# Performance work log

Hardware: AMD Instinct MI355X
Metric: run time of the kernel (lower is better)

The kernel has to match this reference:

```python
import jax, jax.numpy as jnp
import numpy as np

N_NODES = 200000


def gcn_conv(x, src, dst, W, b, num_nodes):
    # PyG GCNConv: add self-loops, symmetric deg^-1/2 normalization,
    # message = norm * (x W)[src], aggregate = scatter-add onto dst, + bias.
    h = x @ W  # [N, out]
    loop = jnp.arange(num_nodes, dtype=src.dtype)
    s = jnp.concatenate([src, loop])
    d = jnp.concatenate([dst, loop])
    deg = jax.ops.segment_sum(jnp.ones_like(d, dtype=h.dtype), d, num_segments=num_nodes)
    dinv = jnp.where(deg > 0, jax.lax.rsqrt(deg), 0.0)
    norm = dinv[s] * dinv[d]  # [E+N]
    msg = h[s] * norm[:, None]  # gather + scale
    out = jax.ops.segment_sum(msg, d, num_segments=num_nodes)  # scatter-add
    return out + b


def setup_inputs() -> dict:
    key = jax.random.key(0)
    k1, k2, k3, k4, k5 = jax.random.split(key, 5)
    x = jax.random.normal(k1, (N_NODES, 3), dtype=jnp.float32)
    edge_index = jax.random.randint(k2, (2, 6400000), 0, N_NODES, dtype=jnp.int64)
    # Glorot-style init for GCN weights, zero bias (PyG defaults)
    W1 = jax.random.normal(k3, (3, 16), dtype=jnp.float32) * (1.0 / np.sqrt(3.0))
    b1 = jnp.zeros((16,), dtype=jnp.float32)
    W2 = jax.random.normal(k4, (16, 1), dtype=jnp.float32) * (1.0 / np.sqrt(16.0))
    b2 = jnp.zeros((1,), dtype=jnp.float32)
    return {"x": x, "edge_index": edge_index, "W1": W1, "b1": b1, "W2": W2, "b2": b2}


def reference(x, edge_index, W1, b1, W2, b2):
    src, dst = edge_index[0], edge_index[1]
    h = gcn_conv(x, src, dst, W1, b1, N_NODES)
    h = jax.nn.relu(h)
    return gcn_conv(h, src, dst, W2, b2, N_NODES)
```

## Files before the change

kernel.cpp:

```cpp
#include <hip/hip_runtime.h>

#define BLK 256
#define PSH 11
#define PART 2048
#define GHB 1024
#define MAXB 256
#define S1SCALE 2097152.0f
#define S2SCALE 524288.0f


__device__ __forceinline__ int edge_at(const void* idx, int is64, long long pos) {
  return is64 ? (int)((const long long*)idx)[pos] : ((const int*)idx)[pos];
}

__global__ void k_detect(const unsigned* __restrict__ w, int* __restrict__ flag) {
  __shared__ int any;
  if (threadIdx.x == 0) any = 0;
  __syncthreads();
  if (w[2 * threadIdx.x + 1] != 0u) atomicOr(&any, 1);
  __syncthreads();
  if (threadIdx.x == 0) *flag = (any == 0) ? 1 : 0;
}


__global__ __launch_bounds__(BLK) void k_hist(const void* __restrict__ ei,
                                              const int* __restrict__ flag,
                                              int E, int chunk, int NB,
                                              int* __restrict__ hist) {
  __shared__ int cnt[MAXB];
  for (int j = threadIdx.x; j < NB; j += BLK) cnt[j] = 0;
  __syncthreads();
  int is64 = *flag;
  int beg = blockIdx.x * chunk, end = min(E, beg + chunk);
  int i = beg + (int)threadIdx.x;
  for (; i + 3 * BLK < end; i += 4 * BLK) {
    int d0 = edge_at(ei, is64, (long long)E + i);
    int d1 = edge_at(ei, is64, (long long)E + i + BLK);
    int d2 = edge_at(ei, is64, (long long)E + i + 2 * BLK);
    int d3 = edge_at(ei, is64, (long long)E + i + 3 * BLK);
    atomicAdd(&cnt[d0 >> PSH], 1);
    atomicAdd(&cnt[d1 >> PSH], 1);
    atomicAdd(&cnt[d2 >> PSH], 1);
    atomicAdd(&cnt[d3 >> PSH], 1);
  }
  for (; i < end; i += BLK)
    atomicAdd(&cnt[edge_at(ei, is64, (long long)E + i) >> PSH], 1);
  __syncthreads();
  int* row = hist + (size_t)blockIdx.x * NB;
  for (int j = threadIdx.x; j < NB; j += BLK) row[j] = cnt[j];
}

__global__ __launch_bounds__(BLK) void k_scan1(int* __restrict__ hist, int NB,
                                               int* __restrict__ btot) {
  const int R = GHB / BLK;
  __shared__ int sd[BLK];
  int b = blockIdx.x, t = threadIdx.x;
  int v[R];
  int sum = 0;
#pragma unroll
  for (int r = 0; r < R; ++r) {
    v[r] = hist[(size_t)(t * R + r) * NB + b];
    sum += v[r];
  }
  sd[t] = sum;
  __syncthreads();
  for (int off = 1; off < BLK; off <<= 1) {
    int tmp = (t >= off) ? sd[t - off] : 0;
    __syncthreads();
    sd[t] += tmp;
    __syncthreads();
  }
  int run = sd[t] - sum;
#pragma unroll
  for (int r = 0; r < R; ++r) {
    int tmp = v[r];
    hist[(size_t)(t * R + r) * NB + b] = run;
    run += tmp;
  }
  if (t == BLK - 1) btot[b] = run;
}

__global__ void k_scan2(const int* __restrict__ btot, int NB, int* __restrict__ ebstart) {
  __shared__ int s[MAXB];
  for (int j = threadIdx.x; j < NB; j += blockDim.x) s[j] = btot[j];
  __syncthreads();
  if (threadIdx.x == 0) {
    int run = 0;
    for (int j = 0; j < NB; ++j) { ebstart[j] = run; run += s[j]; }
    ebstart[NB] = run;
  }
}

__global__ __launch_bounds__(BLK) void k_part(const void* __restrict__ ei,
                                              const int* __restrict__ flag,
                                              int E, int chunk, int NB,
                                              const int* __restrict__ offs,
                                              const int* __restrict__ ebstart,
                                              int* __restrict__ packed) {
  __shared__ int cnt[MAXB];
  int t = threadIdx.x;
  if (t < NB) cnt[t] = ebstart[t] + offs[(size_t)blockIdx.x * NB + t];
  __syncthreads();
  int is64 = *flag;
  int beg = blockIdx.x * chunk, end = min(E, beg + chunk);
  int i = beg + t;
  for (; i + 3 * BLK < end; i += 4 * BLK) {
    int s0 = edge_at(ei, is64, i);
    int s1 = edge_at(ei, is64, i + BLK);
    int s2 = edge_at(ei, is64, i + 2 * BLK);
    int s3 = edge_at(ei, is64, i + 3 * BLK);
    int d0 = edge_at(ei, is64, (long long)E + i);
    int d1 = edge_at(ei, is64, (long long)E + i + BLK);
    int d2 = edge_at(ei, is64, (long long)E + i + 2 * BLK);
    int d3 = edge_at(ei, is64, (long long)E + i + 3 * BLK);
    int p0 = atomicAdd(&cnt[d0 >> PSH], 1);
    int p1 = atomicAdd(&cnt[d1 >> PSH], 1);
    int p2 = atomicAdd(&cnt[d2 >> PSH], 1);
    int p3 = atomicAdd(&cnt[d3 >> PSH], 1);
    packed[p0] = (s0 << PSH) | (d0 & (PART - 1));
    packed[p1] = (s1 << PSH) | (d1 & (PART - 1));
    packed[p2] = (s2 << PSH) | (d2 & (PART - 1));
    packed[p3] = (s3 << PSH) | (d3 & (PART - 1));
  }
  for (; i < end; i += BLK) {
    int s = edge_at(ei, is64, i);
    int d = edge_at(ei, is64, (long long)E + i);
    int pos = atomicAdd(&cnt[d >> PSH], 1);
    packed[pos] = (s << PSH) | (d & (PART - 1));
  }
}

#define SLICE_BOUNDS(KB_)                                                     \
  int b = blockIdx.x, k = blockIdx.y;                                         \
  int s0 = ebstart[b], len = ebstart[b + 1] - s0;                             \
  int lo = s0 + (int)((long long)len * k / (KB_));                            \
  int hi = s0 + (int)((long long)len * (k + 1) / (KB_));                      \
  int alo = min((lo + 3) & ~3, hi);                                           \
  int nvec = (hi - alo) & ~3;                                                 \
  int tails = alo + nvec;

__global__ __launch_bounds__(BLK) void k_degb(const int* __restrict__ packed,
                                              const int* __restrict__ ebstart,
                                              int N, int DKB, int* __restrict__ degp) {
  __shared__ int cnt[PART];
  for (int j = threadIdx.x; j < PART; j += BLK) cnt[j] = 0;
  __syncthreads();
  SLICE_BOUNDS(DKB)
  int t = threadIdx.x;
  if (t < alo - lo) atomicAdd(&cnt[packed[lo + t] & (PART - 1)], 1);
  for (int base = alo + t * 4; base < tails; base += BLK * 4) {
    int4 q = *(const int4*)(packed + base);
    atomicAdd(&cnt[q.x & (PART - 1)], 1);
    atomicAdd(&cnt[q.y & (PART - 1)], 1);
    atomicAdd(&cnt[q.z & (PART - 1)], 1);
    atomicAdd(&cnt[q.w & (PART - 1)], 1);
  }
  if (t < hi - tails) atomicAdd(&cnt[packed[tails + t] & (PART - 1)], 1);
  __syncthreads();
  int pstart = b << PSH;
  int psize = min(N - pstart, PART);
  int* out = degp + (size_t)k * N + pstart;
  for (int j = threadIdx.x; j < psize; j += BLK) out[j] = cnt[j];
}

__global__ __launch_bounds__(BLK) void k_prepb(const int* __restrict__ degp, int DKB,
                                               int N, const float* __restrict__ x,
                                               int4* __restrict__ gx4i) {
  int n = blockIdx.x * blockDim.x + threadIdx.x;
  if (n >= N) return;
  int deg = 1;
  for (int k = 0; k < DKB; ++k) deg += degp[(size_t)k * N + n];
  float di = rsqrtf((float)deg);
  int4 g;
  g.x = __float2int_rn(di * x[3 * n + 0] * S1SCALE);
  g.y = __float2int_rn(di * x[3 * n + 1] * S1SCALE);
  g.z = __float2int_rn(di * x[3 * n + 2] * S1SCALE);
  g.w = __float_as_int(di);
  gx4i[n] = g;
}

__global__ __launch_bounds__(BLK) void k_s1b(const int* __restrict__ packed,
                                             const int* __restrict__ ebstart,
                                             int N, int S1KB,
                                             const int4* __restrict__ gx4i,
                                             int* __restrict__ p1) {
  __shared__ int acc[3 * PART];
  for (int j = threadIdx.x; j < 3 * PART; j += BLK) acc[j] = 0;
  __syncthreads();
  SLICE_BOUNDS(S1KB)
  int t = threadIdx.x;
  if (t < alo - lo) {
    int e = packed[lo + t];
    int4 g = gx4i[e >> PSH];
    int a = 3 * (e & (PART - 1));
    atomicAdd(&acc[a + 0], g.x);
    atomicAdd(&acc[a + 1], g.y);
    atomicAdd(&acc[a + 2], g.z);
  }
  for (int base = alo + t * 4; base < tails; base += BLK * 4) {
    int4 q = *(const int4*)(packed + base);
    int4 g0 = gx4i[q.x >> PSH];
    int4 g1 = gx4i[q.y >> PSH];
    int4 g2 = gx4i[q.z >> PSH];
    int4 g3 = gx4i[q.w >> PSH];
    int a0 = 3 * (q.x & (PART - 1)), a1 = 3 * (q.y & (PART - 1));
    int a2 = 3 * (q.z & (PART - 1)), a3 = 3 * (q.w & (PART - 1));
    atomicAdd(&acc[a0 + 0], g0.x);
    atomicAdd(&acc[a0 + 1], g0.y);
    atomicAdd(&acc[a0 + 2], g0.z);
    atomicAdd(&acc[a1 + 0], g1.x);
    atomicAdd(&acc[a1 + 1], g1.y);
    atomicAdd(&acc[a1 + 2], g1.z);
    atomicAdd(&acc[a2 + 0], g2.x);
    atomicAdd(&acc[a2 + 1], g2.y);
    atomicAdd(&acc[a2 + 2], g2.z);
    atomicAdd(&acc[a3 + 0], g3.x);
    atomicAdd(&acc[a3 + 1], g3.y);
    atomicAdd(&acc[a3 + 2], g3.z);
  }
  if (t < hi - tails) {
    int e = packed[tails + t];
    int4 g = gx4i[e >> PSH];
    int a = 3 * (e & (PART - 1));
    atomicAdd(&acc[a + 0], g.x);
    atomicAdd(&acc[a + 1], g.y);
    atomicAdd(&acc[a + 2], g.z);
  }
  __syncthreads();
  int pstart = b << PSH;
  int psize = min(N - pstart, PART);
  int* out = p1 + (size_t)k * 3 * N + 3 * pstart;
  for (int j = threadIdx.x; j < 3 * psize; j += BLK) out[j] = acc[j];
}

__global__ __launch_bounds__(BLK) void k_midb(const int* __restrict__ p1, int S1KB,
                                              int N, const int4* __restrict__ gx4i,
                                              const float* __restrict__ W1,
                                              const float* __restrict__ b1,
                                              const float* __restrict__ W2,
                                              int* __restrict__ g2i) {
  int n = blockIdx.x * blockDim.x + threadIdx.x;
  if (n >= N) return;
  int4 g = gx4i[n];
  int A0 = g.x, A1 = g.y, A2 = g.z;
  for (int k = 0; k < S1KB; ++k) {
    const int* pp = p1 + (size_t)k * 3 * N + 3 * n;
    A0 += pp[0]; A1 += pp[1]; A2 += pp[2];
  }
  float di = __int_as_float(g.w);
  float sc = di * (1.0f / S1SCALE);
  float a0 = (float)A0 * sc, a1 = (float)A1 * sc, a2 = (float)A2 * sc;
  float h2 = 0.0f;
#pragma unroll
  for (int k = 0; k < 16; ++k) {
    float o = fmaf(a0, W1[k], fmaf(a1, W1[16 + k], fmaf(a2, W1[32 + k], b1[k])));
    o = fmaxf(o, 0.0f);
    h2 = fmaf(o, W2[k], h2);
  }
  g2i[n] = __float2int_rn(di * h2 * S2SCALE);
}

__global__ __launch_bounds__(BLK) void k_s2b(const int* __restrict__ packed,
                                             const int* __restrict__ ebstart,
                                             int N, int DKB,
                                             const int* __restrict__ g2i,
                                             int* __restrict__ p2) {
  __shared__ int acc[PART];
  for (int j = threadIdx.x; j < PART; j += BLK) acc[j] = 0;
  __syncthreads();
  SLICE_BOUNDS(DKB)
  int t = threadIdx.x;
  if (t < alo - lo) {
    int e = packed[lo + t];
    atomicAdd(&acc[e & (PART - 1)], g2i[e >> PSH]);
  }
  for (int base = alo + t * 4; base < tails; base += BLK * 4) {
    int4 q = *(const int4*)(packed + base);
    int v0 = g2i[q.x >> PSH], v1 = g2i[q.y >> PSH];
    int v2 = g2i[q.z >> PSH], v3 = g2i[q.w >> PSH];
    atomicAdd(&acc[q.x & (PART - 1)], v0);
    atomicAdd(&acc[q.y & (PART - 1)], v1);
    atomicAdd(&acc[q.z & (PART - 1)], v2);
    atomicAdd(&acc[q.w & (PART - 1)], v3);
  }
  if (t < hi - tails) {
    int e = packed[tails + t];
    atomicAdd(&acc[e & (PART - 1)], g2i[e >> PSH]);
  }
  __syncthreads();
  int pstart = b << PSH;
  int psize = min(N - pstart, PART);
  int* out = p2 + (size_t)k * N + pstart;
  for (int j = threadIdx.x; j < psize; j += BLK) out[j] = acc[j];
}

__global__ __launch_bounds__(BLK) void k_finalb(const int* __restrict__ p2, int DKB,
                                                int N, const int* __restrict__ g2i,
                                                const int4* __restrict__ gx4i,
                                                const float* __restrict__ b2,
                                                float* __restrict__ out) {
  int n = blockIdx.x * blockDim.x + threadIdx.x;
  if (n >= N) return;
  int S = g2i[n];
  for (int k = 0; k < DKB; ++k) S += p2[(size_t)k * N + n];
  float di = __int_as_float(gx4i[n].w);
  out[n] = di * ((float)S * (1.0f / S2SCALE)) + b2[0];
}


__global__ void k_zero(float* __restrict__ p, int n) {
  int i = blockIdx.x * blockDim.x + threadIdx.x;
  if (i < n) p[i] = 0.0f;
}

__global__ void k_deg(const void* __restrict__ idx, const int* __restrict__ flag,
                      int E, int* __restrict__ deg) {
  int i = blockIdx.x * blockDim.x + threadIdx.x;
  if (i >= E) return;
  int is64 = *flag;
  atomicAdd(&deg[edge_at(idx, is64, (long long)E + i)], 1);
}

__global__ void k_prep(const float* __restrict__ x, const int* __restrict__ deg,
                       float* __restrict__ dinv, float* __restrict__ gx, int N) {
  int n = blockIdx.x * blockDim.x + threadIdx.x;
  if (n >= N) return;
  float di = rsqrtf((float)(deg[n] + 1));
  dinv[n] = di;
  gx[3 * n + 0] = di * x[3 * n + 0];
  gx[3 * n + 1] = di * x[3 * n + 1];
  gx[3 * n + 2] = di * x[3 * n + 2];
}

__global__ void k_scat1(const void* __restrict__ idx, const int* __restrict__ flag,
                        int E, const float* __restrict__ gx, float* __restrict__ aggx) {
  int i = blockIdx.x * blockDim.x + threadIdx.x;
  if (i >= E) return;
  int is64 = *flag;
  int s = edge_at(idx, is64, i);
  int d = edge_at(idx, is64, (long long)E + i);
  unsafeAtomicAdd(&aggx[3 * d + 0], gx[3 * s + 0]);
  unsafeAtomicAdd(&aggx[3 * d + 1], gx[3 * s + 1]);
  unsafeAtomicAdd(&aggx[3 * d + 2], gx[3 * s + 2]);
}

__global__ void k_mid(const float* __restrict__ aggx, const float* __restrict__ gx,
                      const float* __restrict__ dinv,
                      const float* __restrict__ W1, const float* __restrict__ b1,
                      const float* __restrict__ W2, float* __restrict__ g2, int N) {
  int n = blockIdx.x * blockDim.x + threadIdx.x;
  if (n >= N) return;
  float di = dinv[n];
  float a0 = (aggx[3 * n + 0] + gx[3 * n + 0]) * di;
  float a1 = (aggx[3 * n + 1] + gx[3 * n + 1]) * di;
  float a2 = (aggx[3 * n + 2] + gx[3 * n + 2]) * di;
  float h2 = 0.0f;
#pragma unroll
  for (int k = 0; k < 16; ++k) {
    float o = fmaf(a0, W1[k], fmaf(a1, W1[16 + k], fmaf(a2, W1[32 + k], b1[k])));
    o = fmaxf(o, 0.0f);
    h2 = fmaf(o, W2[k], h2);
  }
  g2[n] = di * h2;
}

__global__ void k_scat2(const void* __restrict__ idx, const int* __restrict__ flag,
                        int E, const float* __restrict__ g2, float* __restrict__ agg2) {
  int i = blockIdx.x * blockDim.x + threadIdx.x;
  if (i >= E) return;
  int is64 = *flag;
  int s = edge_at(idx, is64, i);
  int d = edge_at(idx, is64, (long long)E + i);
  unsafeAtomicAdd(&agg2[d], g2[s]);
}

__global__ void k_final(const float* __restrict__ agg2, const float* __restrict__ g2,
                        const float* __restrict__ dinv, const float* __restrict__ b2,
                        float* __restrict__ out, int N) {
  int n = blockIdx.x * blockDim.x + threadIdx.x;
  if (n >= N) return;
  out[n] = dinv[n] * (agg2[n] + g2[n]) + b2[0];
}


extern "C" void kernel_launch(void* const* d_in, const int* in_sizes, int n_in,
                              void* d_out, int out_size, void* d_ws, size_t ws_size,
                              hipStream_t stream) {
  const float* x  = (const float*)d_in[0];
  const void*  ei = d_in[1];
  const float* W1 = (const float*)d_in[2];
  const float* b1 = (const float*)d_in[3];
  const float* W2 = (const float*)d_in[4];
  const float* b2 = (const float*)d_in[5];
  float* out = (float*)d_out;

  const int N = in_sizes[0] / 3;
  const int E = in_sizes[1] / 2;
  const int NB = (N + PART - 1) >> PSH;

  char* ws = (char*)d_ws;
  int gN = (N + BLK - 1) / BLK;
  int gE = (E + BLK - 1) / BLK;

  size_t cur = 0;
  auto take = [&](size_t bytes) { size_t o = cur; cur += (bytes + 255) & ~(size_t)255; return (void*)(ws + o); };
  int*   flag    = (int*)take(256);
  int*   ebstart = (int*)take((size_t)(MAXB + 1) * 4);
  int*   btot    = (int*)take((size_t)MAXB * 4);
  int*   hist    = (int*)take((size_t)GHB * NB * 4);
  int*   packed  = (int*)take((size_t)E * 4);
  int4*  gx4i    = (int4*)take((size_t)N * 16);
  int*   g2i     = (int*)take((size_t)N * 4);
  size_t fixed = cur;

  int s1kb = 16;
  while (s1kb > 4 && fixed + (size_t)s1kb * 3 * N * 4 > ws_size) s1kb -= 4;
  while (s1kb > 1 && fixed + (size_t)s1kb * 3 * N * 4 > ws_size) s1kb >>= 1;

  if (fixed + (size_t)s1kb * 3 * N * 4 <= ws_size && NB <= MAXB) {
    int* partial = (int*)take((size_t)s1kb * 3 * N * 4);
    int dkb = 3 * s1kb; if (dkb > 32) dkb = 32;
    int chunk = (E + GHB - 1) / GHB;

    k_detect<<<1, 256, 0, stream>>>((const unsigned*)ei, flag);
    k_hist<<<GHB, BLK, 0, stream>>>(ei, flag, E, chunk, NB, hist);
    k_scan1<<<NB, BLK, 0, stream>>>(hist, NB, btot);
    k_scan2<<<1, 256, 0, stream>>>(btot, NB, ebstart);
    k_part<<<GHB, BLK, 0, stream>>>(ei, flag, E, chunk, NB, hist, ebstart, packed);
    k_degb<<<dim3(NB, dkb), BLK, 0, stream>>>(packed, ebstart, N, dkb, partial);
    k_prepb<<<gN, BLK, 0, stream>>>((const int*)partial, dkb, N, x, gx4i);
    k_s1b<<<dim3(NB, s1kb), BLK, 0, stream>>>(packed, ebstart, N, s1kb, (const int4*)gx4i, partial);
    k_midb<<<gN, BLK, 0, stream>>>(partial, s1kb, N, (const int4*)gx4i, W1, b1, W2, g2i);
    k_s2b<<<dim3(NB, dkb), BLK, 0, stream>>>(packed, ebstart, N, dkb, (const int*)g2i, partial);
    k_finalb<<<gN, BLK, 0, stream>>>(partial, dkb, N, (const int*)g2i, (const int4*)gx4i, b2, out);
  } else {
    int*   deg   = (int*)(ws + 256);
    float* aggx  = (float*)(ws + 256 + 4ll * N);
    float* agg2b = (float*)(ws + 256 + 4ll * N * 4);
    float* dinvf = (float*)(ws + 256 + 4ll * N * 5);
    float* gx    = (float*)(ws + 256 + 4ll * N * 6);
    float* g2f   = (float*)(ws + 256 + 4ll * N * 9);

    int gZ = (5 * N + BLK - 1) / BLK;

    k_detect<<<1, 256, 0, stream>>>((const unsigned*)ei, (int*)ws);
    k_zero<<<gZ, BLK, 0, stream>>>((float*)deg, 5 * N);
    k_deg<<<gE, BLK, 0, stream>>>(ei, (int*)ws, E, deg);
    k_prep<<<gN, BLK, 0, stream>>>(x, deg, dinvf, gx, N);
    k_scat1<<<gE, BLK, 0, stream>>>(ei, (int*)ws, E, gx, aggx);
    k_mid<<<gN, BLK, 0, stream>>>(aggx, gx, dinvf, W1, b1, W2, g2f, N);
    k_scat2<<<gE, BLK, 0, stream>>>(ei, (int*)ws, E, g2f, agg2b);
    k_final<<<gN, BLK, 0, stream>>>(agg2b, g2f, dinvf, b2, out, N);
  }
}
```

Measured before the change: 162.9 us.

## Stage partition scatter in shared memory to coalesce bucket writes

Adds a write-combining partition kernel that sorts each 2048-edge batch by destination bucket in LDS. It then writes each bucket's run contiguously to global memory, replacing scattered per-edge global stores. This costs extra syncs and a small prefix scan per batch, and the old kernel's unroll was dropped. The chunk size is rounded up to a multiple of 4.

```diff
diff --git a/kernel.cpp b/kernel.cpp
--- a/kernel.cpp
+++ b/kernel.cpp
@@ -5,6 +5,7 @@
 #define PART 2048
 #define GHB 1024
 #define MAXB 256
+#define BATCH 2048
 #define S1SCALE 2097152.0f
 #define S2SCALE 524288.0f
 
@@ -91,6 +92,73 @@
   }
 }
 
+__global__ __launch_bounds__(BLK) void k_part_wc(const void* __restrict__ ei,
+                                                 const int* __restrict__ flag,
+                                                 int E, int chunk, int NB,
+                                                 const int* __restrict__ offs,
+                                                 const int* __restrict__ ebstart,
+                                                 int* __restrict__ packed) {
+  __shared__ int gcur[128];
+  __shared__ int bcnt[128];
+  __shared__ int bbase[128];
+  __shared__ int sc[128];
+  __shared__ int stage[BATCH];
+  __shared__ unsigned char stgb[BATCH];
+  const int t = threadIdx.x;
+  if (t < NB) gcur[t] = ebstart[t] + offs[(size_t)blockIdx.x * NB + t];
+  int is64 = *flag;
+  int beg = blockIdx.x * chunk, end = min(E, beg + chunk);
+  const int U = BATCH / BLK;
+
+  for (int bb = beg; bb < end; bb += BATCH) {
+    int bend = min(end, bb + BATCH);
+    int len = bend - bb;
+    for (int j = t; j < NB; j += BLK) bcnt[j] = 0;
+    __syncthreads();
+    int myb[U], myr[U], myv[U];
+#pragma unroll
+    for (int u = 0; u < U; ++u) {
+      int i = bb + u * BLK + t;
+      myb[u] = -1;
+      if (i < bend) {
+        int s = edge_at(ei, is64, i);
+        int d = edge_at(ei, is64, (long long)E + i);
+        int b = d >> PSH;
+        myb[u] = b;
+        myv[u] = (s << PSH) | (d & (PART - 1));
+        myr[u] = atomicAdd(&bcnt[b], 1);
+      }
+    }
+    __syncthreads();
+    if (t < 128) sc[t] = (t < NB) ? bcnt[t] : 0;
+    __syncthreads();
+    for (int off = 1; off < 128; off <<= 1) {
+      int v = (t < 128 && t >= off) ? sc[t - off] : 0;
+      __syncthreads();
+      if (t < 128) sc[t] += v;
+      __syncthreads();
+    }
+    if (t < NB) bbase[t] = sc[t] - bcnt[t];
+    __syncthreads();
+#pragma unroll
+    for (int u = 0; u < U; ++u) {
+      if (myb[u] >= 0) {
+        int p = bbase[myb[u]] + myr[u];
+        stage[p] = myv[u];
+        stgb[p] = (unsigned char)myb[u];
+      }
+    }
+    __syncthreads();
+    for (int j = t; j < len; j += BLK) {
+      int b = stgb[j];
+      packed[gcur[b] + (j - bbase[b])] = stage[j];
+    }
+    __syncthreads();
+    for (int j = t; j < NB; j += BLK) gcur[j] += bcnt[j];
+    __syncthreads();
+  }
+}
+
 __global__ __launch_bounds__(BLK) void k_part(const void* __restrict__ ei,
                                               const int* __restrict__ flag,
                                               int E, int chunk, int NB,
@@ -103,26 +171,7 @@
   __syncthreads();
   int is64 = *flag;
   int beg = blockIdx.x * chunk, end = min(E, beg + chunk);
-  int i = beg + t;
-  for (; i + 3 * BLK < end; i += 4 * BLK) {
-    int s0 = edge_at(ei, is64, i);
-    int s1 = edge_at(ei, is64, i + BLK);
-    int s2 = edge_at(ei, is64, i + 2 * BLK);
-    int s3 = edge_at(ei, is64, i + 3 * BLK);
-    int d0 = edge_at(ei, is64, (long long)E + i);
-    int d1 = edge_at(ei, is64, (long long)E + i + BLK);
-    int d2 = edge_at(ei, is64, (long long)E + i + 2 * BLK);
-    int d3 = edge_at(ei, is64, (long long)E + i + 3 * BLK);
-    int p0 = atomicAdd(&cnt[d0 >> PSH], 1);
-    int p1 = atomicAdd(&cnt[d1 >> PSH], 1);
-    int p2 = atomicAdd(&cnt[d2 >> PSH], 1);
-    int p3 = atomicAdd(&cnt[d3 >> PSH], 1);
-    packed[p0] = (s0 << PSH) | (d0 & (PART - 1));
-    packed[p1] = (s1 << PSH) | (d1 & (PART - 1));
-    packed[p2] = (s2 << PSH) | (d2 & (PART - 1));
-    packed[p3] = (s3 << PSH) | (d3 & (PART - 1));
-  }
-  for (; i < end; i += BLK) {
+  for (int i = beg + t; i < end; i += BLK) {
     int s = edge_at(ei, is64, i);
     int d = edge_at(ei, is64, (long long)E + i);
     int pos = atomicAdd(&cnt[d >> PSH], 1);
@@ -420,13 +469,16 @@
   if (fixed + (size_t)s1kb * 3 * N * 4 <= ws_size && NB <= MAXB) {
     int* partial = (int*)take((size_t)s1kb * 3 * N * 4);
     int dkb = 3 * s1kb; if (dkb > 32) dkb = 32;
-    int chunk = (E + GHB - 1) / GHB;
+    int chunk = (((E + GHB - 1) / GHB) + 3) & ~3;
 
     k_detect<<<1, 256, 0, stream>>>((const unsigned*)ei, flag);
     k_hist<<<GHB, BLK, 0, stream>>>(ei, flag, E, chunk, NB, hist);
     k_scan1<<<NB, BLK, 0, stream>>>(hist, NB, btot);
     k_scan2<<<1, 256, 0, stream>>>(btot, NB, ebstart);
-    k_part<<<GHB, BLK, 0, stream>>>(ei, flag, E, chunk, NB, hist, ebstart, packed);
+    if (NB <= 128)
+      k_part_wc<<<GHB, BLK, 0, stream>>>(ei, flag, E, chunk, NB, hist, ebstart, packed);
+    else
+      k_part<<<GHB, BLK, 0, stream>>>(ei, flag, E, chunk, NB, hist, ebstart, packed);
     k_degb<<<dim3(NB, dkb), BLK, 0, stream>>>(packed, ebstart, N, dkb, partial);
     k_prepb<<<gN, BLK, 0, stream>>>((const int*)partial, dkb, N, x, gx4i);
     k_s1b<<<dim3(NB, s1kb), BLK, 0, stream>>>(packed, ebstart, N, s1kb, (const int4*)gx4i, partial);
```

After: 160.1 us. About the same (-1.7%).
